# Performance work log

Hardware: AMD Instinct MI355X
Metric: run time of the kernel (lower is better)

The kernel has to match this reference:

```python
import jax, jax.numpy as jnp
import numpy as np

D_MODEL = 1024
EPS = 1e-5  # torch LayerNorm default


def layernorm(x, gamma, beta):
    mu = jnp.mean(x, axis=-1, keepdims=True)
    var = jnp.mean(jnp.square(x - mu), axis=-1, keepdims=True)
    return (x - mu) * jax.lax.rsqrt(var + EPS) * gamma + beta


def setup_inputs() -> dict:
    key = jax.random.key(0)
    ks = jax.random.split(key, 9)
    B, S, D = 4, 2048, D_MODEL
    s = 1.0 / np.sqrt(D)  # ~ nn.Linear default init scale
    return {
        "x": jax.random.normal(ks[0], (B, S, D), dtype=jnp.float32),
        "wq_w": jax.random.uniform(ks[1], (D, D), jnp.float32, -s, s),
        "wq_b": jax.random.uniform(ks[2], (D,), jnp.float32, -s, s),
        "wk_w": jax.random.uniform(ks[3], (D, D), jnp.float32, -s, s),
        "wk_b": jax.random.uniform(ks[4], (D,), jnp.float32, -s, s),
        "wv_w": jax.random.uniform(ks[5], (D, D), jnp.float32, -s, s),
        "wv_b": jax.random.uniform(ks[6], (D,), jnp.float32, -s, s),
        "lin_w": jax.random.uniform(ks[7], (D, D), jnp.float32, -s, s),
        "lin_b": jax.random.uniform(ks[8], (D,), jnp.float32, -s, s),
        "g1": jnp.ones((D,), jnp.float32),
        "b1": jnp.zeros((D,), jnp.float32),
        "g2": jnp.ones((D,), jnp.float32),
        "b2": jnp.zeros((D,), jnp.float32),
    }


def reference(x, wq_w, wq_b, wk_w, wk_b, wv_w, wv_b, lin_w, lin_b, g1, b1, g2, b2):
    # single-head attention over full d_model (num_heads unused in original forward)
    q = jnp.einsum("bsd,ed->bse", x, wq_w) + wq_b
    k = jnp.einsum("bsd,ed->bse", x, wk_w) + wk_b
    v = jnp.einsum("bsd,ed->bse", x, wv_w) + wv_b
    scale = 1.0 / jnp.sqrt(jnp.float32(x.shape[-1]))
    scores = jax.nn.softmax(jnp.einsum("bqd,bkd->bqk", q, k) * scale, axis=2)
    attention = jnp.einsum("bqk,bkd->bqd", scores, v)
    # faithful to original: tril applied to the [S, D] attention OUTPUT per batch
    attention = jnp.tril(attention)
    x = layernorm(x + attention, g1, b1)
    linear_output = jnp.einsum("bsd,ed->bse", x, lin_w) + lin_b
    x = layernorm(x + linear_output, g2, b2)
    return x
```

## Files before the change

### kernel.cpp

```cpp
#include <hip/hip_runtime.h>
#include <hip/hip_bf16.h>

#define SEQ 2048
#define DM 1024
#define NB 4

typedef short bf16x8 __attribute__((ext_vector_type(8)));
typedef float f32x4 __attribute__((ext_vector_type(4)));
typedef float f32x4v __attribute__((ext_vector_type(4)));
typedef unsigned short u16x4 __attribute__((ext_vector_type(4)));
typedef unsigned short u16x8 __attribute__((ext_vector_type(8)));

__device__ __forceinline__ float bf2f(unsigned short u) {
  union { unsigned int i; float f; } w; w.i = ((unsigned int)u) << 16; return w.f;
}
__device__ __forceinline__ unsigned short f2bf(float f) {
  union { __hip_bfloat16 h; unsigned short u; } w; w.h = __float2bfloat16(f); return w.u;
}
__device__ __forceinline__ void load_lds16(const void* g, void* l) {
  __builtin_amdgcn_global_load_lds((const __attribute__((address_space(1))) void*)g,
                                   (__attribute__((address_space(3))) void*)l, 16, 0, 0);
}

__global__ __launch_bounds__(256) void cvt_kernel(const float* __restrict__ in,
                                                  unsigned short* __restrict__ out, int n4) {
  int idx = blockIdx.x * 256 + threadIdx.x;
  int stride = gridDim.x * 256;
  for (int i = idx; i < n4; i += stride) {
    f32x4v x = ((const f32x4v*)in)[i];
    u16x4 o;
    o[0] = f2bf(x[0]); o[1] = f2bf(x[1]); o[2] = f2bf(x[2]); o[3] = f2bf(x[3]);
    ((u16x4*)out)[i] = o;
  }
}

__global__ __launch_bounds__(256, 2) void gemm_bt(
    const unsigned short* __restrict__ A, int lda, long sA,
    const unsigned short* __restrict__ B, int ldb, long sB,
    void* __restrict__ Cv, int ldc, long sC,
    int K, const float* __restrict__ bias, float scale, int outf32, int trilskip)
{
  const int m0 = blockIdx.x * 128, n0 = blockIdx.y * 128;
  if (trilskip && n0 > m0 + 127) return;
  __shared__ unsigned short As[128 * 64];
  __shared__ unsigned short Bs[128 * 64];
  const int tid = threadIdx.x;
  const int lane = tid & 63;
  const int wave = tid >> 6;
  const int wm = wave >> 1, wn = wave & 1;
  const unsigned short* Ab = A + (size_t)sA * blockIdx.z;
  const unsigned short* Bb = B + (size_t)sB * blockIdx.z;

  f32x4 acc[4][4];
#pragma unroll
  for (int i = 0; i < 4; ++i)
#pragma unroll
    for (int j = 0; j < 4; ++j)
      acc[i][j] = (f32x4){0.f, 0.f, 0.f, 0.f};

  const int nk = K >> 6;
  for (int kt = 0; kt < nk; ++kt) {
    __syncthreads();
    const int kb = kt << 6;
#pragma unroll
    for (int it = 0; it < 4; ++it) {
      int c = it * 256 + tid;
      int row = c >> 3;
      int lslot = (c & 7) ^ (row & 7);
      int ldsoff = (it * 256 + wave * 64) * 8;
      load_lds16(Ab + (size_t)(m0 + row) * lda + kb + lslot * 8, &As[ldsoff]);
      load_lds16(Bb + (size_t)(n0 + row) * ldb + kb + lslot * 8, &Bs[ldsoff]);
    }
    __syncthreads();
#pragma unroll
    for (int h = 0; h < 2; ++h) {
      bf16x8 af[4], bfr[4];
#pragma unroll
      for (int i = 0; i < 4; ++i) {
        int row = wm * 64 + i * 16 + (lane & 15);
        int pslot = (h * 4 + (lane >> 4)) ^ (row & 7);
        af[i] = *(const bf16x8*)&As[row * 64 + pslot * 8];
      }
#pragma unroll
      for (int j = 0; j < 4; ++j) {
        int row = wn * 64 + j * 16 + (lane & 15);
        int pslot = (h * 4 + (lane >> 4)) ^ (row & 7);
        bfr[j] = *(const bf16x8*)&Bs[row * 64 + pslot * 8];
      }
#pragma unroll
      for (int i = 0; i < 4; ++i)
#pragma unroll
        for (int j = 0; j < 4; ++j)
          acc[i][j] = __builtin_amdgcn_mfma_f32_16x16x32_bf16(af[i], bfr[j], acc[i][j], 0, 0, 0);
    }
  }

  const int rsub = (lane >> 4) * 4;
  const int cbase = n0 + wn * 64 + (lane & 15);
  if (outf32) {
    float* C = (float*)Cv + (size_t)sC * blockIdx.z;
#pragma unroll
    for (int i = 0; i < 4; ++i) {
      int rbase = m0 + wm * 64 + i * 16 + rsub;
#pragma unroll
      for (int j = 0; j < 4; ++j)
#pragma unroll
        for (int r = 0; r < 4; ++r)
          C[(size_t)(rbase + r) * ldc + cbase + j * 16] = acc[i][j][r] * scale;
    }
  } else {
    unsigned short* C = (unsigned short*)Cv + (size_t)sC * blockIdx.z;
    float bv[4] = {0.f, 0.f, 0.f, 0.f};
    if (bias) {
#pragma unroll
      for (int j = 0; j < 4; ++j) bv[j] = bias[cbase + j * 16];
    }
#pragma unroll
    for (int i = 0; i < 4; ++i) {
      int rbase = m0 + wm * 64 + i * 16 + rsub;
#pragma unroll
      for (int j = 0; j < 4; ++j)
#pragma unroll
        for (int r = 0; r < 4; ++r)
          C[(size_t)(rbase + r) * ldc + cbase + j * 16] = f2bf(acc[i][j][r] * scale + bv[j]);
    }
  }
}

__global__ __launch_bounds__(512, 2) void gemm256(
    const unsigned short* __restrict__ A, int lda, long sA,
    const unsigned short* __restrict__ B, int ldb, long sB,
    void* __restrict__ Cv, int ldc, long sC,
    int K, const float* __restrict__ bias, float scale, int outf32)
{
  __shared__ unsigned short As[2][256 * 64];
  __shared__ unsigned short Bs[2][256 * 64];
  const int tid = threadIdx.x;
  const int lane = tid & 63;
  const int wave = tid >> 6;
  const int wm = wave >> 2;
  const int wn = wave & 3;
  const int m0 = blockIdx.x * 256, n0 = blockIdx.y * 256;
  const unsigned short* Ab = A + (size_t)sA * blockIdx.z;
  const unsigned short* Bb = B + (size_t)sB * blockIdx.z;

  f32x4 acc[8][4];
#pragma unroll
  for (int i = 0; i < 8; ++i)
#pragma unroll
    for (int j = 0; j < 4; ++j)
      acc[i][j] = (f32x4){0.f, 0.f, 0.f, 0.f};

  const int nk = K >> 6;

  auto STAGE = [&](int b, int kt) {
    const int kb = kt << 6;
#pragma unroll
    for (int i = 0; i < 4; ++i) {
      int c = i * 512 + tid;
      int row = c >> 3;
      int lslot = (c & 7) ^ (row & 7);
      load_lds16(Ab + (size_t)(m0 + row) * lda + kb + lslot * 8, &As[b][c * 8]);
      load_lds16(Bb + (size_t)(n0 + row) * ldb + kb + lslot * 8, &Bs[b][c * 8]);
    }
  };

  STAGE(0, 0);
  if (nk > 1) {
    STAGE(1, 1);
    asm volatile("s_waitcnt vmcnt(8)" ::: "memory");
  } else {
    asm volatile("s_waitcnt vmcnt(0)" ::: "memory");
  }
  __builtin_amdgcn_sched_barrier(0);
  __builtin_amdgcn_s_barrier();
  __builtin_amdgcn_sched_barrier(0);

  for (int kt = 0; kt < nk; ++kt) {
    const int b = kt & 1;
    const unsigned short* Asb = As[b];
    const unsigned short* Bsb = Bs[b];
    bf16x8 bfr[4][2];
#pragma unroll
    for (int j = 0; j < 4; ++j) {
      int row = wn * 64 + j * 16 + (lane & 15);
#pragma unroll
      for (int h = 0; h < 2; ++h) {
        int pslot = (h * 4 + (lane >> 4)) ^ (row & 7);
        bfr[j][h] = *(const bf16x8*)&Bsb[row * 64 + pslot * 8];
      }
    }
#pragma unroll
    for (int q = 0; q < 4; ++q) {
      bf16x8 af[2][2];
#pragma unroll
      for (int i = 0; i < 2; ++i) {
        int row = wm * 128 + (q * 2 + i) * 16 + (lane & 15);
#pragma unroll
        for (int h = 0; h < 2; ++h) {
          int pslot = (h * 4 + (lane >> 4)) ^ (row & 7);
          af[i][h] = *(const bf16x8*)&Asb[row * 64 + pslot * 8];
        }
      }
      __builtin_amdgcn_s_setprio(1);
#pragma unroll
      for (int i = 0; i < 2; ++i)
#pragma unroll
        for (int j = 0; j < 4; ++j)
#pragma unroll
          for (int h = 0; h < 2; ++h)
            acc[q * 2 + i][j] =
                __builtin_amdgcn_mfma_f32_16x16x32_bf16(af[i][h], bfr[j][h], acc[q * 2 + i][j], 0, 0, 0);
      __builtin_amdgcn_s_setprio(0);
    }
    __builtin_amdgcn_sched_barrier(0);
    __builtin_amdgcn_s_barrier();
    __builtin_amdgcn_sched_barrier(0);
    if (kt + 2 < nk) STAGE(b, kt + 2);
    if (kt + 1 < nk) {
      if (kt + 2 < nk) asm volatile("s_waitcnt vmcnt(8)" ::: "memory");
      else             asm volatile("s_waitcnt vmcnt(0)" ::: "memory");
      __builtin_amdgcn_sched_barrier(0);
      __builtin_amdgcn_s_barrier();
      __builtin_amdgcn_sched_barrier(0);
    }
  }

  const int rsub = (lane >> 4) * 4;
  const int cbase = n0 + wn * 64 + (lane & 15);
  if (outf32) {
    float* C = (float*)Cv + (size_t)sC * blockIdx.z;
#pragma unroll
    for (int i = 0; i < 8; ++i) {
      int rbase = m0 + wm * 128 + i * 16 + rsub;
#pragma unroll
      for (int j = 0; j < 4; ++j)
#pragma unroll
        for (int r = 0; r < 4; ++r)
          C[(size_t)(rbase + r) * ldc + cbase + j * 16] = acc[i][j][r] * scale;
    }
  } else {
    unsigned short* C = (unsigned short*)Cv + (size_t)sC * blockIdx.z;
    float bv[4] = {0.f, 0.f, 0.f, 0.f};
    if (bias) {
#pragma unroll
      for (int j = 0; j < 4; ++j) bv[j] = bias[cbase + j * 16];
    }
#pragma unroll
    for (int i = 0; i < 8; ++i) {
      int rbase = m0 + wm * 128 + i * 16 + rsub;
#pragma unroll
      for (int j = 0; j < 4; ++j)
#pragma unroll
        for (int r = 0; r < 4; ++r)
          C[(size_t)(rbase + r) * ldc + cbase + j * 16] = f2bf(acc[i][j][r] * scale + bv[j]);
    }
  }
}

__global__ __launch_bounds__(256) void transpose_kernel(const unsigned short* __restrict__ v,
                                                        int lda, long sV,
                                                        unsigned short* __restrict__ vt) {
  __shared__ unsigned short t[64][65];
  int b = blockIdx.z;
  int s0 = blockIdx.x * 64;
  int d0 = blockIdx.y * 64;
  int tid = threadIdx.x;
  int rr = tid >> 3;
  int c8 = (tid & 7) * 8;
  const unsigned short* vb = v + (size_t)sV * b;
#pragma unroll
  for (int it = 0; it < 2; ++it) {
    int row = rr + it * 32;
    u16x8 val = *(const u16x8*)&vb[(size_t)(s0 + row) * lda + d0 + c8];
#pragma unroll
    for (int j = 0; j < 8; ++j) t[row][c8 + j] = val[j];
  }
  __syncthreads();
#pragma unroll
  for (int it = 0; it < 2; ++it) {
    int drow = rr + it * 32;
    u16x8 o;
#pragma unroll
    for (int j = 0; j < 8; ++j) o[j] = t[c8 + j][drow];
    *(u16x8*)&vt[((size_t)b * DM + d0 + drow) * SEQ + s0 + c8] = o;
  }
}

__global__ __launch_bounds__(256) void softmax_kernel(unsigned short* __restrict__ Sc) {
  int row = blockIdx.x;
  int tid = threadIdx.x;
  unsigned short* sr = Sc + (size_t)row * SEQ;
  u16x8 raw = *(const u16x8*)&sr[tid * 8];
  float v[8];
#pragma unroll
  for (int j = 0; j < 8; ++j) v[j] = bf2f(raw[j]);
  float m = v[0];
#pragma unroll
  for (int j = 1; j < 8; ++j) m = fmaxf(m, v[j]);
#pragma unroll
  for (int off = 32; off; off >>= 1) m = fmaxf(m, __shfl_xor(m, off));
  __shared__ float red[8];
  int wv = tid >> 6;
  if ((tid & 63) == 0) red[wv] = m;
  __syncthreads();
  m = fmaxf(fmaxf(red[0], red[1]), fmaxf(red[2], red[3]));
  float s = 0.f;
#pragma unroll
  for (int j = 0; j < 8; ++j) { v[j] = __expf(v[j] - m); s += v[j]; }
#pragma unroll
  for (int off = 32; off; off >>= 1) s += __shfl_xor(s, off);
  if ((tid & 63) == 0) red[4 + wv] = s;
  __syncthreads();
  s = red[4] + red[5] + red[6] + red[7];
  float inv = 1.f / s;
  u16x8 o;
#pragma unroll
  for (int j = 0; j < 8; ++j) o[j] = f2bf(v[j] * inv);
  *(u16x8*)&sr[tid * 8] = o;
}

__global__ __launch_bounds__(256) void ln_kernel(
    const float* __restrict__ xf, const unsigned short* __restrict__ xb,
    const unsigned short* __restrict__ res, int masked,
    const float* __restrict__ g, const float* __restrict__ be,
    float* __restrict__ outf, unsigned short* __restrict__ outb)
{
  int row = blockIdx.x;
  int s = row & (SEQ - 1);
  int tid = threadIdx.x;
  int d0 = tid * 4;
  float v[4];
  if (xf) {
    f32x4v t = ((const f32x4v*)(xf + (size_t)row * DM))[tid];
    v[0]=t[0]; v[1]=t[1]; v[2]=t[2]; v[3]=t[3];
  } else {
    u16x4 t = ((const u16x4*)(xb + (size_t)row * DM))[tid];
    v[0]=bf2f(t[0]); v[1]=bf2f(t[1]); v[2]=bf2f(t[2]); v[3]=bf2f(t[3]);
  }
  u16x4 rv = ((const u16x4*)(res + (size_t)row * DM))[tid];
#pragma unroll
  for (int j = 0; j < 4; ++j) {
    float r = bf2f(rv[j]);
    if (masked && (d0 + j) > s) r = 0.f;
    v[j] += r;
  }
  float s1 = v[0] + v[1] + v[2] + v[3];
  float s2 = v[0]*v[0] + v[1]*v[1] + v[2]*v[2] + v[3]*v[3];
#pragma unroll
  for (int off = 32; off; off >>= 1) { s1 += __shfl_xor(s1, off); s2 += __shfl_xor(s2, off); }
  __shared__ float red[8];
  int wv = tid >> 6;
  if ((tid & 63) == 0) { red[wv] = s1; red[4 + wv] = s2; }
  __syncthreads();
  s1 = red[0] + red[1] + red[2] + red[3];
  s2 = red[4] + red[5] + red[6] + red[7];
  float mean = s1 * (1.f / DM);
  float var = s2 * (1.f / DM) - mean * mean;
  float rstd = rsqrtf(var + 1e-5f);
  f32x4v gv = ((const f32x4v*)g)[tid];
  f32x4v bv = ((const f32x4v*)be)[tid];
  if (outf) {
    f32x4v o;
#pragma unroll
    for (int j = 0; j < 4; ++j) o[j] = (v[j] - mean) * rstd * gv[j] + bv[j];
    ((f32x4v*)(outf + (size_t)row * DM))[tid] = o;
  } else {
    u16x4 o;
#pragma unroll
    for (int j = 0; j < 4; ++j) o[j] = f2bf((v[j] - mean) * rstd * gv[j] + bv[j]);
    ((u16x4*)(outb + (size_t)row * DM))[tid] = o;
  }
}

extern "C" void kernel_launch(void* const* d_in, const int* in_sizes, int n_in,
                              void* d_out, int out_size, void* d_ws, size_t ws_size,
                              hipStream_t stream) {
  (void)in_sizes; (void)n_in; (void)out_size; (void)ws_size;
  const float* x     = (const float*)d_in[0];
  const float* wq_w  = (const float*)d_in[1];
  const float* wq_b  = (const float*)d_in[2];
  const float* wk_w  = (const float*)d_in[3];
  const float* wk_b  = (const float*)d_in[4];
  const float* wv_w  = (const float*)d_in[5];
  const float* wv_b  = (const float*)d_in[6];
  const float* lin_w = (const float*)d_in[7];
  const float* lin_b = (const float*)d_in[8];
  const float* g1    = (const float*)d_in[9];
  const float* b1    = (const float*)d_in[10];
  const float* g2    = (const float*)d_in[11];
  const float* b2    = (const float*)d_in[12];

  const size_t MB = 1ull << 20;
  char* ws = (char*)d_ws;
  unsigned short* scP  = (unsigned short*)(ws);
  unsigned short* attn = (unsigned short*)(ws + 32*MB);
  unsigned short* x1   = (unsigned short*)(ws + 48*MB);
  unsigned short* lin  = (unsigned short*)(ws + 64*MB);
  unsigned short* xb   = (unsigned short*)(ws + 80*MB);
  unsigned short* wqkvb= (unsigned short*)(ws + 96*MB);
  unsigned short* lwb  = (unsigned short*)(ws + 102*MB);
  float*          bqkv = (float*)(ws + 104*MB);
  unsigned short* qkv  = (unsigned short*)(ws + 112*MB);
  unsigned short* vt   = (unsigned short*)(ws + 160*MB);

  const size_t SD = (size_t)NB * SEQ * DM;

  cvt_kernel<<<2048, 256, 0, stream>>>(x, xb, (int)(SD / 4));
  cvt_kernel<<<1024, 256, 0, stream>>>(wq_w, wqkvb, DM * DM / 4);
  cvt_kernel<<<1024, 256, 0, stream>>>(wk_w, wqkvb + DM * DM, DM * DM / 4);
  cvt_kernel<<<1024, 256, 0, stream>>>(wv_w, wqkvb + 2 * DM * DM, DM * DM / 4);
  cvt_kernel<<<1024, 256, 0, stream>>>(lin_w, lwb, DM * DM / 4);
  hipMemcpyAsync(bqkv,        wq_b, DM * sizeof(float), hipMemcpyDeviceToDevice, stream);
  hipMemcpyAsync(bqkv + DM,   wk_b, DM * sizeof(float), hipMemcpyDeviceToDevice, stream);
  hipMemcpyAsync(bqkv + 2*DM, wv_b, DM * sizeof(float), hipMemcpyDeviceToDevice, stream);

  gemm_bt<<<dim3(64, 24, 1), 256, 0, stream>>>(xb, DM, 0, wqkvb, DM, 0, qkv, 3 * DM, 0,
                                               DM, bqkv, 1.f, 0, 0);
  transpose_kernel<<<dim3(SEQ / 64, DM / 64, NB), 256, 0, stream>>>(
      qkv + 2 * DM, 3 * DM, (long)SEQ * 3 * DM, vt);

  const float scale = 0.03125f;
  gemm256<<<dim3(8, 8, NB), 512, 0, stream>>>(
      qkv, 3 * DM, (long)SEQ * 3 * DM,
      qkv + DM, 3 * DM, (long)SEQ * 3 * DM,
      scP, SEQ, (long)SEQ * SEQ, DM, nullptr, scale, 0);
  softmax_kernel<<<NB * SEQ, 256, 0, stream>>>(scP);
  gemm_bt<<<dim3(16, 8, NB), 256, 0, stream>>>(
      scP, SEQ, (long)SEQ * SEQ,
      vt, SEQ, (long)DM * SEQ,
      attn, DM, (long)SEQ * DM, SEQ, nullptr, 1.f, 0, 1);

  ln_kernel<<<NB * SEQ, 256, 0, stream>>>(x, nullptr, attn, 1, g1, b1, nullptr, x1);
  gemm_bt<<<dim3(64, 8, 1), 256, 0, stream>>>(x1, DM, 0, lwb, DM, 0, lin, DM, 0, DM, lin_b, 1.f, 0, 0);
  ln_kernel<<<NB * SEQ, 256, 0, stream>>>(nullptr, x1, lin, 0, g2, b2, (float*)d_out, nullptr);
}
```

Baseline: 235.2 us.

## Fuse input conversions, move QKV GEMM to 256-tile kernel with transposed V epilogue

Merges the five cast kernels and three bias memcpys into one staging kernel. Runs the QKV projection on the double-buffered 256x256 GEMM and writes the V columns directly in transposed layout, which removes the separate transpose kernel. The first layernorm now reads the bf16 copy of x instead of the fp32 input, cutting its input traffic but changing the residual's precision. The transposed stores are 4-element strided writes, which may coalesce poorly.

```diff
diff --git a/kernel.cpp b/kernel.cpp
--- a/kernel.cpp
+++ b/kernel.cpp
@@ -21,16 +21,39 @@
   __builtin_amdgcn_global_load_lds((const __attribute__((address_space(1))) void*)g,
                                    (__attribute__((address_space(3))) void*)l, 16, 0, 0);
 }
-
-__global__ __launch_bounds__(256) void cvt_kernel(const float* __restrict__ in,
-                                                  unsigned short* __restrict__ out, int n4) {
+__device__ __forceinline__ void cvt4(const float* __restrict__ in,
+                                     unsigned short* __restrict__ out, int i) {
+  f32x4v v = ((const f32x4v*)in)[i];
+  u16x4 o;
+  o[0] = f2bf(v[0]); o[1] = f2bf(v[1]); o[2] = f2bf(v[2]); o[3] = f2bf(v[3]);
+  ((u16x4*)out)[i] = o;
+}
+
+__global__ __launch_bounds__(256) void stage_kernel(
+    const float* __restrict__ x,
+    const float* __restrict__ wq, const float* __restrict__ wk,
+    const float* __restrict__ wv, const float* __restrict__ lw,
+    const float* __restrict__ bq, const float* __restrict__ bk, const float* __restrict__ bv,
+    unsigned short* __restrict__ xb, unsigned short* __restrict__ wqkvb,
+    unsigned short* __restrict__ lwb, float* __restrict__ bqkv)
+{
+  const int XC = (NB * SEQ * DM) / 4;
+  const int WC = (DM * DM) / 4;
+  const int BC = (3 * DM) / 4;
+  const int total = XC + 4 * WC + BC;
   int idx = blockIdx.x * 256 + threadIdx.x;
   int stride = gridDim.x * 256;
-  for (int i = idx; i < n4; i += stride) {
-    f32x4v x = ((const f32x4v*)in)[i];
-    u16x4 o;
-    o[0] = f2bf(x[0]); o[1] = f2bf(x[1]); o[2] = f2bf(x[2]); o[3] = f2bf(x[3]);
-    ((u16x4*)out)[i] = o;
+  for (int i = idx; i < total; i += stride) {
+    if (i < XC) { cvt4(x, xb, i); continue; }
+    int j = i - XC;
+    if (j < WC)          { cvt4(wq, wqkvb, j); continue; }
+    if (j < 2 * WC)      { cvt4(wk, wqkvb + (size_t)DM * DM, j - WC); continue; }
+    if (j < 3 * WC)      { cvt4(wv, wqkvb + 2 * (size_t)DM * DM, j - 2 * WC); continue; }
+    if (j < 4 * WC)      { cvt4(lw, lwb, j - 3 * WC); continue; }
+    int c = j - 4 * WC;
+    const float* src = (c < 256) ? bq : ((c < 512) ? bk : bv);
+    int off = (c < 256) ? c : ((c < 512) ? c - 256 : c - 512);
+    ((f32x4v*)bqkv)[c] = ((const f32x4v*)src)[off];
   }
 }
 
@@ -131,7 +154,8 @@
     const unsigned short* __restrict__ A, int lda, long sA,
     const unsigned short* __restrict__ B, int ldb, long sB,
     void* __restrict__ Cv, int ldc, long sC,
-    int K, const float* __restrict__ bias, float scale, int outf32)
+    int K, const float* __restrict__ bias, float scale, int outf32,
+    unsigned short* __restrict__ vtOut, int vtBase)
 {
   __shared__ unsigned short As[2][256 * 64];
   __shared__ unsigned short Bs[2][256 * 64];
@@ -228,7 +252,27 @@
 
   const int rsub = (lane >> 4) * 4;
   const int cbase = n0 + wn * 64 + (lane & 15);
-  if (outf32) {
+  if (vtOut && n0 >= vtBase) {
+    float bv[4] = {0.f, 0.f, 0.f, 0.f};
+    if (bias) {
+#pragma unroll
+      for (int j = 0; j < 4; ++j) bv[j] = bias[cbase + j * 16];
+    }
+#pragma unroll
+    for (int i = 0; i < 8; ++i) {
+      int sg = m0 + wm * 128 + i * 16 + rsub;
+      int bb = sg >> 11;
+      int sl = sg & (SEQ - 1);
+#pragma unroll
+      for (int j = 0; j < 4; ++j) {
+        int d = cbase + j * 16 - vtBase;
+        u16x4 o;
+#pragma unroll
+        for (int r = 0; r < 4; ++r) o[r] = f2bf(acc[i][j][r] * scale + bv[j]);
+        *(u16x4*)&vtOut[((size_t)bb * DM + d) * SEQ + sl] = o;
+      }
+    }
+  } else if (outf32) {
     float* C = (float*)Cv + (size_t)sC * blockIdx.z;
 #pragma unroll
     for (int i = 0; i < 8; ++i) {
@@ -255,35 +299,6 @@
         for (int r = 0; r < 4; ++r)
           C[(size_t)(rbase + r) * ldc + cbase + j * 16] = f2bf(acc[i][j][r] * scale + bv[j]);
     }
-  }
-}
-
-__global__ __launch_bounds__(256) void transpose_kernel(const unsigned short* __restrict__ v,
-                                                        int lda, long sV,
-                                                        unsigned short* __restrict__ vt) {
-  __shared__ unsigned short t[64][65];
-  int b = blockIdx.z;
-  int s0 = blockIdx.x * 64;
-  int d0 = blockIdx.y * 64;
-  int tid = threadIdx.x;
-  int rr = tid >> 3;
-  int c8 = (tid & 7) * 8;
-  const unsigned short* vb = v + (size_t)sV * b;
-#pragma unroll
-  for (int it = 0; it < 2; ++it) {
-    int row = rr + it * 32;
-    u16x8 val = *(const u16x8*)&vb[(size_t)(s0 + row) * lda + d0 + c8];
-#pragma unroll
-    for (int j = 0; j < 8; ++j) t[row][c8 + j] = val[j];
-  }
-  __syncthreads();
-#pragma unroll
-  for (int it = 0; it < 2; ++it) {
-    int drow = rr + it * 32;
-    u16x8 o;
-#pragma unroll
-    for (int j = 0; j < 8; ++j) o[j] = t[c8 + j][drow];
-    *(u16x8*)&vt[((size_t)b * DM + d0 + drow) * SEQ + s0 + c8] = o;
   }
 }
 
@@ -404,34 +419,24 @@
   unsigned short* qkv  = (unsigned short*)(ws + 112*MB);
   unsigned short* vt   = (unsigned short*)(ws + 160*MB);
 
-  const size_t SD = (size_t)NB * SEQ * DM;
-
-  cvt_kernel<<<2048, 256, 0, stream>>>(x, xb, (int)(SD / 4));
-  cvt_kernel<<<1024, 256, 0, stream>>>(wq_w, wqkvb, DM * DM / 4);
-  cvt_kernel<<<1024, 256, 0, stream>>>(wk_w, wqkvb + DM * DM, DM * DM / 4);
-  cvt_kernel<<<1024, 256, 0, stream>>>(wv_w, wqkvb + 2 * DM * DM, DM * DM / 4);
-  cvt_kernel<<<1024, 256, 0, stream>>>(lin_w, lwb, DM * DM / 4);
-  hipMemcpyAsync(bqkv,        wq_b, DM * sizeof(float), hipMemcpyDeviceToDevice, stream);
-  hipMemcpyAsync(bqkv + DM,   wk_b, DM * sizeof(float), hipMemcpyDeviceToDevice, stream);
-  hipMemcpyAsync(bqkv + 2*DM, wv_b, DM * sizeof(float), hipMemcpyDeviceToDevice, stream);
-
-  gemm_bt<<<dim3(64, 24, 1), 256, 0, stream>>>(xb, DM, 0, wqkvb, DM, 0, qkv, 3 * DM, 0,
-                                               DM, bqkv, 1.f, 0, 0);
-  transpose_kernel<<<dim3(SEQ / 64, DM / 64, NB), 256, 0, stream>>>(
-      qkv + 2 * DM, 3 * DM, (long)SEQ * 3 * DM, vt);
+  stage_kernel<<<2048, 256, 0, stream>>>(x, wq_w, wk_w, wv_w, lin_w, wq_b, wk_b, wv_b,
+                                         xb, wqkvb, lwb, bqkv);
+
+  gemm256<<<dim3(32, 12, 1), 512, 0, stream>>>(xb, DM, 0, wqkvb, DM, 0, qkv, 3 * DM, 0,
+                                               DM, bqkv, 1.f, 0, vt, 2 * DM);
 
   const float scale = 0.03125f;
   gemm256<<<dim3(8, 8, NB), 512, 0, stream>>>(
       qkv, 3 * DM, (long)SEQ * 3 * DM,
       qkv + DM, 3 * DM, (long)SEQ * 3 * DM,
-      scP, SEQ, (long)SEQ * SEQ, DM, nullptr, scale, 0);
+      scP, SEQ, (long)SEQ * SEQ, DM, nullptr, scale, 0, nullptr, 0);
   softmax_kernel<<<NB * SEQ, 256, 0, stream>>>(scP);
   gemm_bt<<<dim3(16, 8, NB), 256, 0, stream>>>(
       scP, SEQ, (long)SEQ * SEQ,
       vt, SEQ, (long)DM * SEQ,
       attn, DM, (long)SEQ * DM, SEQ, nullptr, 1.f, 0, 1);
 
-  ln_kernel<<<NB * SEQ, 256, 0, stream>>>(x, nullptr, attn, 1, g1, b1, nullptr, x1);
+  ln_kernel<<<NB * SEQ, 256, 0, stream>>>(nullptr, xb, attn, 1, g1, b1, nullptr, x1);
   gemm_bt<<<dim3(64, 8, 1), 256, 0, stream>>>(x1, DM, 0, lwb, DM, 0, lin, DM, 0, DM, lin_b, 1.f, 0, 0);
   ln_kernel<<<NB * SEQ, 256, 0, stream>>>(nullptr, x1, lin, 0, g2, b2, (float*)d_out, nullptr);
 }
```

New measurement: 224.4 us. 4.6% less time.
